# Kernel tuning notes

Measured on AMD Instinct MI355X. Metric: run time of the kernel, lower is better.

The kernel has to match this reference:

```python
import jax, jax.numpy as jnp
import numpy as np

H = 64          # hidden_size / SINDy latent dim
DM = 128        # d_model (GRU input size)
FF = 128        # dim_feedforward
NL = 2          # num_sindy_layers
EPS = 1e-5      # LayerNorm eps (torch default)
TRI_I, TRI_J = np.triu_indices(H)          # poly_order=2 pairs, torch loop order (i<=j)
LIB = 1 + H + TRI_I.size                   # 2145


def layernorm(x, g, b):
    m = jnp.mean(x, axis=-1, keepdims=True)
    v = jnp.mean((x - m) ** 2, axis=-1, keepdims=True)
    return (x - m) * jax.lax.rsqrt(v + EPS) * g + b


def sindy_library(z):
    # z: (N, H) -> Theta: (N, 1 + H + H*(H+1)/2); same term ordering as torch loops
    ones = jnp.ones((z.shape[0], 1), z.dtype)
    quad = z[:, TRI_I] * z[:, TRI_J]
    return jnp.concatenate([ones, z, quad], axis=1)


def gru_layer(x, Wih, Whh, bih, bhh):
    # x: (B, S, in), Wih: (3H, in), Whh: (3H, H); torch GRU gate order r,z,n
    xp = jnp.einsum('bsi,gi->bsg', x, Wih) + bih  # (B,S,3H) precomputed input projections
    B = x.shape[0]

    def step(h, xpt):
        gh = h @ Whh.T + bhh
        r = jax.nn.sigmoid(xpt[:, :H] + gh[:, :H])
        z = jax.nn.sigmoid(xpt[:, H:2 * H] + gh[:, H:2 * H])
        n = jnp.tanh(xpt[:, 2 * H:] + r * gh[:, 2 * H:])
        h = (1.0 - z) * n + z * h
        return h, h

    h0 = jnp.zeros((B, H), x.dtype)
    _, ys = jax.lax.scan(step, h0, jnp.swapaxes(xp, 0, 1))  # scan over time
    return jnp.swapaxes(ys, 0, 1)  # (B, S, H)


def sindy_layer(src, coef, g1, b1n, W1, bf1, W2, bf2, g2, b2n):
    B, S, _ = src.shape
    theta = sindy_library(src.reshape(-1, H))          # (N, LIB)
    upd = (theta @ coef).reshape(B, S, H)              # (B, S, H)
    src = layernorm(src + upd, g1, b1n)                # dropout = identity (eval)
    ff = jax.nn.gelu(src @ W1.T + bf1, approximate=False) @ W2.T + bf2
    return layernorm(src + ff, g2, b2n)


def setup_inputs() -> dict:
    key = jax.random.key(0)
    ks = jax.random.split(key, 24)
    f = lambda k, sh, s=0.05: (jax.random.normal(k, sh, dtype=jnp.float32) * s)
    inp = {
        'x': jax.random.normal(ks[0], (32, 500, DM), dtype=jnp.float32),
        # GRU layer 0 (input DM) and layer 1 (input H)
        'Wih0': f(ks[1], (3 * H, DM)), 'Whh0': f(ks[2], (3 * H, H)),
        'bih0': f(ks[3], (3 * H,)), 'bhh0': f(ks[4], (3 * H,)),
        'Wih1': f(ks[5], (3 * H, H)), 'Whh1': f(ks[6], (3 * H, H)),
        'bih1': f(ks[7], (3 * H,)), 'bhh1': f(ks[8], (3 * H,)),
        # stacked params for NL=2 identical SINDy layers
        'coeffs': f(ks[9], (NL, LIB, H), 0.02),
        'ln1_g': jnp.ones((NL, H), jnp.float32), 'ln1_b': jnp.zeros((NL, H), jnp.float32),
        'W1': f(ks[10], (NL, FF, H)), 'b1': f(ks[11], (NL, FF)),
        'W2': f(ks[12], (NL, H, FF)), 'b2': f(ks[13], (NL, H)),
        'ln2_g': jnp.ones((NL, H), jnp.float32), 'ln2_b': jnp.zeros((NL, H), jnp.float32),
    }
    return inp


def reference(x, Wih0, Whh0, bih0, bhh0, Wih1, Whh1, bih1, bhh1,
              coeffs, ln1_g, ln1_b, W1, b1, W2, b2, ln2_g, ln2_b):
    h = gru_layer(x, Wih0, Whh0, bih0, bhh0)
    h = gru_layer(h, Wih1, Whh1, bih1, bhh1)
    for l in range(NL):
        h = sindy_layer(h, coeffs[l], ln1_g[l], ln1_b[l], W1[l], b1[l],
                        W2[l], b2[l], ln2_g[l], ln2_b[l])
    return h, h[:, -1, :]
```

## Files before the change

### kernel.cpp

```cpp
#include <hip/hip_runtime.h>
#include <hip/hip_bf16.h>
#include <math.h>

#define H 64
#define DM 128
#define GDIM 192
#define BSZ 32
#define SEQ 500
#define NROW (BSZ*SEQ)
#define LIBN 2145
#define FFD 128
#define KPAD 2176
#define NKC 68

typedef __attribute__((ext_vector_type(8))) short short8;
typedef __attribute__((ext_vector_type(4))) float f32x4;
typedef __attribute__((ext_vector_type(4))) unsigned u32x4;

__device__ __forceinline__ float sigf(float x) {
    return 1.0f / (1.0f + __expf(-x));
}
__device__ __forceinline__ float tanhfast(float x) {
    x = fminf(fmaxf(x, -15.0f), 15.0f);
    float t = __expf(-2.0f * x);
    return (1.0f - t) / (1.0f + t);
}
__device__ __forceinline__ short bf16r(float f) {
    unsigned u = __float_as_uint(f);
    unsigned r = (u + 0x7fffu + ((u >> 16) & 1u)) >> 16;
    return (short)r;
}

__global__ void pack_wih0(const float* __restrict__ w, float* __restrict__ wt) {
    int idx = blockIdx.x * 256 + threadIdx.x;
    if (idx >= GDIM * DM) return;
    int e  = idx & 3;
    int g  = (idx >> 2) % GDIM;
    int k4 = idx / (GDIM * 4);
    wt[idx] = w[g * DM + k4 * 4 + e];
}

__global__ void pack_coef_frag(const float* __restrict__ coef, short* __restrict__ cp) {
    int idx = blockIdx.x * 256 + threadIdx.x;
    int j = idx & 7, lane = (idx >> 3) & 63, nt = (idx >> 9) & 3, kc = idx >> 11;
    int k = kc * 32 + ((lane >> 4) << 3) + j;
    int c = nt * 16 + (lane & 15);
    float v = (k < LIBN) ? coef[(size_t)k * H + c] : 0.0f;
    cp[idx] = bf16r(v);
}
__global__ void pack_w1_frag(const float* __restrict__ w1, short* __restrict__ wp) {
    int idx = blockIdx.x * 256 + threadIdx.x;
    int j = idx & 7, lane = (idx >> 3) & 63, nt = (idx >> 9) & 7, kc = idx >> 12;
    int k = kc * 32 + ((lane >> 4) << 3) + j;
    int n = nt * 16 + (lane & 15);
    wp[idx] = bf16r(w1[(size_t)n * H + k]);
}
__global__ void pack_w2_frag(const float* __restrict__ w2, short* __restrict__ wp) {
    int idx = blockIdx.x * 256 + threadIdx.x;
    int j = idx & 7, lane = (idx >> 3) & 63, nt = (idx >> 9) & 3, kc = idx >> 11;
    int k = kc * 32 + ((lane >> 4) << 3) + j;
    int n = nt * 16 + (lane & 15);
    wp[idx] = bf16r(w2[(size_t)n * FFD + k]);
}

__global__ __launch_bounds__(192, 2) void xp0_gemm(const float* __restrict__ x,
                                                   const float* __restrict__ wtp,
                                                   const float* __restrict__ bih0,
                                                   float* __restrict__ xp0) {
    __shared__ float xs[64][DM];
    int rb = blockIdx.x * 64;
    for (int idx = threadIdx.x; idx < 64 * 32; idx += 192) {
        int r = idx >> 5, k4 = idx & 31;
        ((f32x4*)xs[r])[k4] = ((const f32x4*)(x + (size_t)(rb + r) * DM))[k4];
    }
    __syncthreads();
    int g = threadIdx.x;
    float bias = bih0[g];
    float acc[64];
#pragma unroll
    for (int r = 0; r < 64; r++) acc[r] = bias;
    for (int k4 = 0; k4 < 32; k4++) {
        f32x4 w4 = ((const f32x4*)wtp)[k4 * GDIM + g];
#pragma unroll
        for (int r = 0; r < 64; r++) {
            f32x4 xv = ((f32x4*)xs[r])[k4];
            acc[r] += w4[0] * xv[0] + w4[1] * xv[1] + w4[2] * xv[2] + w4[3] * xv[3];
        }
    }
    for (int r = 0; r < 64; r++) xp0[(size_t)(rb + r) * GDIM + g] = acc[r];
}

__global__ __launch_bounds__(768, 3) void gru_fused(const float* __restrict__ xp0,
                                                    const float* __restrict__ whh0,
                                                    const float* __restrict__ bhh0,
                                                    const float* __restrict__ wih1,
                                                    const float* __restrict__ bih1,
                                                    const float* __restrict__ whh1,
                                                    const float* __restrict__ bhh1,
                                                    float* __restrict__ hbuf) {
    int b = blockIdx.x;
    int tid = threadIdx.x;
    int wv = __builtin_amdgcn_readfirstlane(tid >> 6);
    int lane = tid & 63;
    int m = wv % 3;
    int q = wv / 3;
    int k0 = q * 16;

    __shared__ __align__(16) float h0s[H];
    __shared__ __align__(16) float h1s[H];
    __shared__ float part[3][4][GDIM];

    if (tid < H) { h0s[tid] = 0.0f; h1s[tid] = 0.0f; }

    const float* W = (m == 0) ? whh0 : (m == 1) ? wih1 : whh1;
    float wr[16], wz[16], wn[16];
#pragma unroll
    for (int k4 = 0; k4 < 4; k4++) {
        f32x4 a = ((const f32x4*)(W + (size_t)lane * H + k0))[k4];
        f32x4 c = ((const f32x4*)(W + (size_t)(H + lane) * H + k0))[k4];
        f32x4 d = ((const f32x4*)(W + (size_t)(2 * H + lane) * H + k0))[k4];
        wr[4*k4] = a[0]; wr[4*k4+1] = a[1]; wr[4*k4+2] = a[2]; wr[4*k4+3] = a[3];
        wz[4*k4] = c[0]; wz[4*k4+1] = c[1]; wz[4*k4+2] = c[2]; wz[4*k4+3] = c[3];
        wn[4*k4] = d[0]; wn[4*k4+1] = d[1]; wn[4*k4+2] = d[2]; wn[4*k4+3] = d[3];
    }

    float b0r = 0, b0z = 0, b0n = 0;
    float b1ir = 0, b1iz = 0, b1in = 0, b1hr = 0, b1hz = 0, b1hn = 0;
    float hreg0 = 0.0f, hreg1 = 0.0f;
    const float* xpb = xp0 + (size_t)b * SEQ * GDIM;
    float xr_c = 0, xz_c = 0, xn_c = 0, xr_n = 0, xz_n = 0, xn_n = 0;
    if (wv == 0) {
        b0r = bhh0[lane]; b0z = bhh0[H + lane]; b0n = bhh0[2 * H + lane];
        xr_c = xpb[lane]; xz_c = xpb[H + lane]; xn_c = xpb[2 * H + lane];
    } else if (wv == 2) {
        b1ir = bih1[lane]; b1iz = bih1[H + lane]; b1in = bih1[2 * H + lane];
        b1hr = bhh1[lane]; b1hz = bhh1[H + lane]; b1hn = bhh1[2 * H + lane];
    }
    __syncthreads();

    for (int s = 0; s <= SEQ; s++) {
        if (wv == 0 && s + 1 < SEQ) {
            const float* p = xpb + (size_t)(s + 1) * GDIM;
            xr_n = p[lane]; xz_n = p[H + lane]; xn_n = p[2 * H + lane];
        }
        const float* hv = (m == 2) ? h1s : h0s;
        float ar = 0, az = 0, an = 0;
#pragma unroll
        for (int t4 = 0; t4 < 4; t4++) {
            f32x4 h4 = ((const f32x4*)(hv + k0))[t4];
            ar += wr[4*t4] * h4[0] + wr[4*t4+1] * h4[1] + wr[4*t4+2] * h4[2] + wr[4*t4+3] * h4[3];
            az += wz[4*t4] * h4[0] + wz[4*t4+1] * h4[1] + wz[4*t4+2] * h4[2] + wz[4*t4+3] * h4[3];
            an += wn[4*t4] * h4[0] + wn[4*t4+1] * h4[1] + wn[4*t4+2] * h4[2] + wn[4*t4+3] * h4[3];
        }
        part[m][q][lane] = ar;
        part[m][q][H + lane] = az;
        part[m][q][2 * H + lane] = an;
        __syncthreads();

        if (wv == 0) {
            if (s < SEQ) {
                float gr = b0r, gz = b0z, gn = b0n;
#pragma unroll
                for (int qq = 0; qq < 4; qq++) {
                    gr += part[0][qq][lane];
                    gz += part[0][qq][H + lane];
                    gn += part[0][qq][2 * H + lane];
                }
                float rg = sigf(xr_c + gr);
                float zg = sigf(xz_c + gz);
                float ng = tanhfast(xn_c + rg * gn);
                hreg0 = (1.0f - zg) * ng + zg * hreg0;
                h0s[lane] = hreg0;
                xr_c = xr_n; xz_c = xz_n; xn_c = xn_n;
            }
        } else if (wv == 2) {
            if (s >= 1) {
                float xr1 = b1ir, xz1 = b1iz, xn1 = b1in;
                float gr1 = b1hr, gz1 = b1hz, gn1 = b1hn;
#pragma unroll
                for (int qq = 0; qq < 4; qq++) {
                    xr1 += part[1][qq][lane];
                    xz1 += part[1][qq][H + lane];
                    xn1 += part[1][qq][2 * H + lane];
                    gr1 += part[2][qq][lane];
                    gz1 += part[2][qq][H + lane];
                    gn1 += part[2][qq][2 * H + lane];
                }
                float rg = sigf(xr1 + gr1);
                float zg = sigf(xz1 + gz1);
                float ng = tanhfast(xn1 + rg * gn1);
                hreg1 = (1.0f - zg) * ng + zg * hreg1;
                h1s[lane] = hreg1;
                hbuf[((size_t)b * SEQ + (s - 1)) * H + lane] = hreg1;
            }
        }
        __syncthreads();
    }
}

__global__ __launch_bounds__(512) void sindy_mfma(float* __restrict__ hbuf,
                                                  const short* __restrict__ cpk,
                                                  const short* __restrict__ w1p,
                                                  const short* __restrict__ w2p,
                                                  const float* __restrict__ g1,
                                                  const float* __restrict__ b1n,
                                                  const float* __restrict__ bf1,
                                                  const float* __restrict__ bf2v,
                                                  const float* __restrict__ g2,
                                                  const float* __restrict__ b2n,
                                                  float* __restrict__ out,
                                                  int final_layer) {
    __shared__ float z[64 * 68];
    __shared__ float upd[64 * 68];
    __shared__ float ff[64 * 132];
    __shared__ unsigned kmap[KPAD];
    __shared__ float bfs1[FFD], bfs2[H], g1s[H], b1s[H], g2s[H], b2s[H];

    int tid = threadIdx.x;
    int wv = __builtin_amdgcn_readfirstlane(tid >> 6);
    int lane = tid & 63;
    int row0 = blockIdx.x * 64;

    for (int idx = tid; idx < 64 * 16; idx += 512) {
        int r = idx >> 4, c4 = idx & 15;
        *(f32x4*)&z[r * 68 + c4 * 4] = *(const f32x4*)&hbuf[(size_t)(row0 + r) * H + c4 * 4];
    }
    for (int idx = tid; idx < 64 * 17; idx += 512)
        *(f32x4*)&upd[idx * 4] = (f32x4){0.f, 0.f, 0.f, 0.f};
    if (tid < 64) {
        z[tid * 68 + 64] = 1.0f; z[tid * 68 + 65] = 0.0f;
        z[tid * 68 + 66] = 0.0f; z[tid * 68 + 67] = 0.0f;
    }
    for (int k = tid; k < KPAD; k += 512) {
        unsigned a, b;
        if (k == 0) { a = 64; b = 64; }
        else if (k < 1 + H) { a = (unsigned)(k - 1); b = 64; }
        else if (k < LIBN) {
            int q = k - (1 + H);
            double s = sqrt(16641.0 - 8.0 * (double)q);
            int i = (int)((129.0 - s) * 0.5);
            int base = 64 * i - (i * (i - 1)) / 2;
            a = (unsigned)i; b = (unsigned)(i + (q - base));
        } else { a = 65; b = 65; }
        kmap[k] = (a << 16) | b;
    }
    if (tid < FFD) bfs1[tid] = bf1[tid];
    if (tid < H) {
        bfs2[tid] = bf2v[tid];
        g1s[tid] = g1[tid]; b1s[tid] = b1n[tid];
        g2s[tid] = g2[tid]; b2s[tid] = b2n[tid];
    }
    __syncthreads();

    int kj0 = ((lane >> 4) << 3);
    int m0 = (wv & 3) * 16;
    int m = m0 + (lane & 15);
    int rbase = m0 + ((lane >> 4) << 2);
    int cb16 = lane & 15;
    const float* zrow = &z[m * 68];

    {
        int p = wv >> 2;
        f32x4 acc[4] = {{0,0,0,0},{0,0,0,0},{0,0,0,0},{0,0,0,0}};
        for (int kc = p; kc < NKC; kc += 2) {
            int kbase = kc * 32 + kj0;
            u32x4 km0 = *(const u32x4*)&kmap[kbase];
            u32x4 km1 = *(const u32x4*)&kmap[kbase + 4];
            short8 af;
            af[0] = bf16r(zrow[km0[0] >> 16] * zrow[km0[0] & 0xffff]);
            af[1] = bf16r(zrow[km0[1] >> 16] * zrow[km0[1] & 0xffff]);
            af[2] = bf16r(zrow[km0[2] >> 16] * zrow[km0[2] & 0xffff]);
            af[3] = bf16r(zrow[km0[3] >> 16] * zrow[km0[3] & 0xffff]);
            af[4] = bf16r(zrow[km1[0] >> 16] * zrow[km1[0] & 0xffff]);
            af[5] = bf16r(zrow[km1[1] >> 16] * zrow[km1[1] & 0xffff]);
            af[6] = bf16r(zrow[km1[2] >> 16] * zrow[km1[2] & 0xffff]);
            af[7] = bf16r(zrow[km1[3] >> 16] * zrow[km1[3] & 0xffff]);
            const short* cb = cpk + ((size_t)(kc * 4) * 64 + lane) * 8;
#pragma unroll
            for (int nt = 0; nt < 4; nt++) {
                short8 bf = *(const short8*)(cb + (size_t)nt * 512);
                acc[nt] = __builtin_amdgcn_mfma_f32_16x16x32_bf16(af, bf, acc[nt], 0, 0, 0);
            }
        }
#pragma unroll
        for (int nt = 0; nt < 4; nt++)
#pragma unroll
            for (int r = 0; r < 4; r++)
                atomicAdd(&upd[(rbase + r) * 68 + nt * 16 + cb16], acc[nt][r]);
    }
    __syncthreads();

    if (wv == 0) {
        float v[64];
        float s1 = 0.0f;
#pragma unroll
        for (int c = 0; c < 64; c++) { v[c] = z[lane * 68 + c] + upd[lane * 68 + c]; s1 += v[c]; }
        float mn = s1 * (1.0f / 64.0f);
        float s2 = 0.0f;
#pragma unroll
        for (int c = 0; c < 64; c++) { float d = v[c] - mn; s2 += d * d; }
        float rstd = 1.0f / sqrtf(s2 * (1.0f / 64.0f) + 1e-5f);
#pragma unroll
        for (int c = 0; c < 64; c++)
            z[lane * 68 + c] = (v[c] - mn) * rstd * g1s[c] + b1s[c];
    }
    __syncthreads();

    {
        int nq = wv >> 2;
        f32x4 acc[4] = {{0,0,0,0},{0,0,0,0},{0,0,0,0},{0,0,0,0}};
#pragma unroll
        for (int kc = 0; kc < 2; kc++) {
            f32x4 za = *(const f32x4*)&z[m * 68 + kc * 32 + kj0];
            f32x4 zb = *(const f32x4*)&z[m * 68 + kc * 32 + kj0 + 4];
            short8 af;
            af[0] = bf16r(za[0]); af[1] = bf16r(za[1]); af[2] = bf16r(za[2]); af[3] = bf16r(za[3]);
            af[4] = bf16r(zb[0]); af[5] = bf16r(zb[1]); af[6] = bf16r(zb[2]); af[7] = bf16r(zb[3]);
#pragma unroll
            for (int t = 0; t < 4; t++) {
                int nt = nq * 4 + t;
                short8 bf = *(const short8*)(w1p + ((size_t)(kc * 8 + nt) * 64 + lane) * 8);
                acc[t] = __builtin_amdgcn_mfma_f32_16x16x32_bf16(af, bf, acc[t], 0, 0, 0);
            }
        }
#pragma unroll
        for (int t = 0; t < 4; t++) {
            int col = (nq * 4 + t) * 16 + cb16;
#pragma unroll
            for (int r = 0; r < 4; r++) {
                float v = acc[t][r] + bfs1[col];
                ff[(rbase + r) * 132 + col] = 0.5f * v * (1.0f + erff(v * 0.70710678118654752f));
            }
        }
    }
    __syncthreads();

    {
        int nh = wv >> 2;
        f32x4 acc[2] = {{0,0,0,0},{0,0,0,0}};
        const float* frow = &ff[m * 132];
#pragma unroll
        for (int kc = 0; kc < 4; kc++) {
            f32x4 fa = *(const f32x4*)&frow[kc * 32 + kj0];
            f32x4 fb = *(const f32x4*)&frow[kc * 32 + kj0 + 4];
            short8 af;
            af[0] = bf16r(fa[0]); af[1] = bf16r(fa[1]); af[2] = bf16r(fa[2]); af[3] = bf16r(fa[3]);
            af[4] = bf16r(fb[0]); af[5] = bf16r(fb[1]); af[6] = bf16r(fb[2]); af[7] = bf16r(fb[3]);
#pragma unroll
            for (int t = 0; t < 2; t++) {
                int nt = nh * 2 + t;
                short8 bf = *(const short8*)(w2p + ((size_t)(kc * 4 + nt) * 64 + lane) * 8);
                acc[t] = __builtin_amdgcn_mfma_f32_16x16x32_bf16(af, bf, acc[t], 0, 0, 0);
            }
        }
#pragma unroll
        for (int t = 0; t < 2; t++) {
            int col = (nh * 2 + t) * 16 + cb16;
#pragma unroll
            for (int r = 0; r < 4; r++)
                upd[(rbase + r) * 68 + col] = acc[t][r] + bfs2[col];
        }
    }
    __syncthreads();

    if (wv == 0) {
        float v[64];
        float s1 = 0.0f;
#pragma unroll
        for (int c = 0; c < 64; c++) { v[c] = z[lane * 68 + c] + upd[lane * 68 + c]; s1 += v[c]; }
        float mn = s1 * (1.0f / 64.0f);
        float s2 = 0.0f;
#pragma unroll
        for (int c = 0; c < 64; c++) { float d = v[c] - mn; s2 += d * d; }
        float rstd = 1.0f / sqrtf(s2 * (1.0f / 64.0f) + 1e-5f);
        int row = row0 + lane;
#pragma unroll
        for (int c = 0; c < 64; c++) {
            float res = (v[c] - mn) * rstd * g2s[c] + b2s[c];
            if (!final_layer) {
                hbuf[(size_t)row * H + c] = res;
            } else {
                out[(size_t)row * H + c] = res;
                if (row % SEQ == SEQ - 1)
                    out[(size_t)NROW * H + (row / SEQ) * H + c] = res;
            }
        }
    }
}

extern "C" void kernel_launch(void* const* d_in, const int* in_sizes, int n_in,
                              void* d_out, int out_size, void* d_ws, size_t ws_size,
                              hipStream_t stream) {
    const float* x    = (const float*)d_in[0];
    const float* wih0 = (const float*)d_in[1];
    const float* whh0 = (const float*)d_in[2];
    const float* bih0 = (const float*)d_in[3];
    const float* bhh0 = (const float*)d_in[4];
    const float* wih1 = (const float*)d_in[5];
    const float* whh1 = (const float*)d_in[6];
    const float* bih1 = (const float*)d_in[7];
    const float* bhh1 = (const float*)d_in[8];
    const float* coeffs = (const float*)d_in[9];
    const float* ln1g = (const float*)d_in[10];
    const float* ln1b = (const float*)d_in[11];
    const float* w1   = (const float*)d_in[12];
    const float* b1   = (const float*)d_in[13];
    const float* w2   = (const float*)d_in[14];
    const float* b2   = (const float*)d_in[15];
    const float* ln2g = (const float*)d_in[16];
    const float* ln2b = (const float*)d_in[17];

    float* out = (float*)d_out;
    float* ws  = (float*)d_ws;
    float* xp0 = ws;
    float* wtp = ws + (size_t)NROW * GDIM;
    short* bfa = (short*)(wtp + GDIM * DM);
    short* cpk[2] = { bfa, bfa + 139264 };
    short* w1pk[2] = { bfa + 2 * 139264, bfa + 2 * 139264 + 8192 };
    short* w2pk[2] = { bfa + 2 * 139264 + 2 * 8192, bfa + 2 * 139264 + 3 * 8192 };
    float* hbuf = out;

    pack_wih0<<<(GDIM * DM + 255) / 256, 256, 0, stream>>>(wih0, wtp);
    for (int l = 0; l < 2; l++) {
        pack_coef_frag<<<139264 / 256, 256, 0, stream>>>(coeffs + (size_t)l * LIBN * H, cpk[l]);
        pack_w1_frag<<<8192 / 256, 256, 0, stream>>>(w1 + (size_t)l * FFD * H, w1pk[l]);
        pack_w2_frag<<<8192 / 256, 256, 0, stream>>>(w2 + (size_t)l * H * FFD, w2pk[l]);
    }
    xp0_gemm<<<NROW / 64, 192, 0, stream>>>(x, wtp, bih0, xp0);
    gru_fused<<<BSZ, 768, 0, stream>>>(xp0, whh0, bhh0, wih1, bih1, whh1, bhh1, hbuf);
    for (int l = 0; l < 2; l++) {
        sindy_mfma<<<NROW / 64, 512, 0, stream>>>(
            hbuf, cpk[l], w1pk[l], w2pk[l],
            ln1g + l * H, ln1b + l * H, b1 + l * FFD,
            b2 + l * H, ln2g + l * H, ln2b + l * H,
            out, l == 1);
    }
}
```

Before: 573.0 us.

## Run GRU recurrence with bf16 MFMA over batches of 16 sequences per block

Replaces the per-sequence fp32 FMA GRU kernel (one block per batch element, 768 threads with partial-sum reduction through shared memory) with a kernel that batches 16 sequences per block and computes the recurrent matvecs as bf16 16x16x32 MFMAs. Weights are pre-packed into MFMA fragment layout, and hidden states are kept double-buffered in shared memory as bf16, which removes one barrier and the partial-sum reduction per step. The trade-off is only 2 blocks for the whole recurrence, so very low GPU occupancy, plus bf16 rounding of the hidden state feeding each step, which adds numerical error that accumulates over 500 steps.

```diff
diff --git a/kernel.cpp b/kernel.cpp
--- a/kernel.cpp
+++ b/kernel.cpp
@@ -12,6 +12,7 @@
 #define FFD 128
 #define KPAD 2176
 #define NKC 68
+#define NB 16
 
 typedef __attribute__((ext_vector_type(8))) short short8;
 typedef __attribute__((ext_vector_type(4))) float f32x4;
@@ -61,6 +62,14 @@
     int k = kc * 32 + ((lane >> 4) << 3) + j;
     int n = nt * 16 + (lane & 15);
     wp[idx] = bf16r(w2[(size_t)n * FFD + k]);
+}
+__global__ void pack_gruw_frag(const float* __restrict__ w, short* __restrict__ wp) {
+    int idx = blockIdx.x * 256 + threadIdx.x;
+    if (idx >= 12288) return;
+    int j = idx & 7, lane = (idx >> 3) & 63, kc = (idx >> 9) & 1, t = idx >> 10;
+    int m = 16 * t + (lane & 15);
+    int k = kc * 32 + ((lane >> 4) << 3) + j;
+    wp[idx] = bf16r(w[(size_t)m * H + k]);
 }
 
 __global__ __launch_bounds__(192, 2) void xp0_gemm(const float* __restrict__ x,
@@ -90,108 +99,137 @@
     for (int r = 0; r < 64; r++) xp0[(size_t)(rb + r) * GDIM + g] = acc[r];
 }
 
-__global__ __launch_bounds__(768, 3) void gru_fused(const float* __restrict__ xp0,
-                                                    const float* __restrict__ whh0,
-                                                    const float* __restrict__ bhh0,
-                                                    const float* __restrict__ wih1,
-                                                    const float* __restrict__ bih1,
-                                                    const float* __restrict__ whh1,
-                                                    const float* __restrict__ bhh1,
-                                                    float* __restrict__ hbuf) {
-    int b = blockIdx.x;
+__global__ __launch_bounds__(512) void gru_mfma(const float* __restrict__ xp0,
+                                                const short* __restrict__ a0,
+                                                const short* __restrict__ a1,
+                                                const short* __restrict__ a2,
+                                                const float* __restrict__ bhh0,
+                                                const float* __restrict__ bih1,
+                                                const float* __restrict__ bhh1,
+                                                float* __restrict__ hbuf) {
+    int n0 = blockIdx.x * NB;
     int tid = threadIdx.x;
     int wv = __builtin_amdgcn_readfirstlane(tid >> 6);
     int lane = tid & 63;
-    int m = wv % 3;
-    int q = wv / 3;
-    int k0 = q * 16;
-
-    __shared__ __align__(16) float h0s[H];
-    __shared__ __align__(16) float h1s[H];
-    __shared__ float part[3][4][GDIM];
-
-    if (tid < H) { h0s[tid] = 0.0f; h1s[tid] = 0.0f; }
-
-    const float* W = (m == 0) ? whh0 : (m == 1) ? wih1 : whh1;
-    float wr[16], wz[16], wn[16];
-#pragma unroll
-    for (int k4 = 0; k4 < 4; k4++) {
-        f32x4 a = ((const f32x4*)(W + (size_t)lane * H + k0))[k4];
-        f32x4 c = ((const f32x4*)(W + (size_t)(H + lane) * H + k0))[k4];
-        f32x4 d = ((const f32x4*)(W + (size_t)(2 * H + lane) * H + k0))[k4];
-        wr[4*k4] = a[0]; wr[4*k4+1] = a[1]; wr[4*k4+2] = a[2]; wr[4*k4+3] = a[3];
-        wz[4*k4] = c[0]; wz[4*k4+1] = c[1]; wz[4*k4+2] = c[2]; wz[4*k4+3] = c[3];
-        wn[4*k4] = d[0]; wn[4*k4+1] = d[1]; wn[4*k4+2] = d[2]; wn[4*k4+3] = d[3];
-    }
-
-    float b0r = 0, b0z = 0, b0n = 0;
-    float b1ir = 0, b1iz = 0, b1in = 0, b1hr = 0, b1hz = 0, b1hn = 0;
-    float hreg0 = 0.0f, hreg1 = 0.0f;
-    const float* xpb = xp0 + (size_t)b * SEQ * GDIM;
-    float xr_c = 0, xz_c = 0, xn_c = 0, xr_n = 0, xz_n = 0, xn_n = 0;
-    if (wv == 0) {
-        b0r = bhh0[lane]; b0z = bhh0[H + lane]; b0n = bhh0[2 * H + lane];
-        xr_c = xpb[lane]; xz_c = xpb[H + lane]; xn_c = xpb[2 * H + lane];
-    } else if (wv == 2) {
-        b1ir = bih1[lane]; b1iz = bih1[H + lane]; b1in = bih1[2 * H + lane];
-        b1hr = bhh1[lane]; b1hz = bhh1[H + lane]; b1hn = bhh1[2 * H + lane];
+    int g = wv >> 2;
+    int w = wv & 3;
+    int quad = lane >> 4;
+    int n = lane & 15;
+    int i0 = 16 * w + quad * 4;
+
+    __shared__ short hb0[2][NB][72];
+    __shared__ short hb1[2][NB][72];
+
+    for (int idx = tid; idx < 2 * NB * 72; idx += 512) {
+        ((short*)hb0)[idx] = 0;
+        ((short*)hb1)[idx] = 0;
+    }
+
+    short8 A0[6], A1[6], A2[6];
+    if (g == 0) {
+#pragma unroll
+        for (int t3 = 0; t3 < 3; t3++)
+#pragma unroll
+            for (int kc = 0; kc < 2; kc++)
+                A0[t3 * 2 + kc] = *(const short8*)(a0 + (((size_t)(w + 4 * t3) * 2 + kc) * 64 + lane) * 8);
+    } else {
+#pragma unroll
+        for (int t3 = 0; t3 < 3; t3++)
+#pragma unroll
+            for (int kc = 0; kc < 2; kc++) {
+                A1[t3 * 2 + kc] = *(const short8*)(a1 + (((size_t)(w + 4 * t3) * 2 + kc) * 64 + lane) * 8);
+                A2[t3 * 2 + kc] = *(const short8*)(a2 + (((size_t)(w + 4 * t3) * 2 + kc) * 64 + lane) * 8);
+            }
+    }
+    float bR[4], bZ[4], bN[4], cR[4], cZ[4], cN[4];
+#pragma unroll
+    for (int r = 0; r < 4; r++) {
+        if (g == 0) {
+            bR[r] = bhh0[i0 + r]; bZ[r] = bhh0[H + i0 + r]; bN[r] = bhh0[2 * H + i0 + r];
+        } else {
+            bR[r] = bih1[i0 + r]; bZ[r] = bih1[H + i0 + r]; bN[r] = bih1[2 * H + i0 + r];
+            cR[r] = bhh1[i0 + r]; cZ[r] = bhh1[H + i0 + r]; cN[r] = bhh1[2 * H + i0 + r];
+        }
+    }
+
+    float hprev[4] = {0.f, 0.f, 0.f, 0.f};
+    const float* xpB = xp0 + (size_t)(n0 + n) * SEQ * GDIM;
+    f32x4 xr_c = {0,0,0,0}, xz_c = {0,0,0,0}, xn_c = {0,0,0,0};
+    f32x4 xr_n = {0,0,0,0}, xz_n = {0,0,0,0}, xn_n = {0,0,0,0};
+    if (g == 0) {
+        xr_c = *(const f32x4*)(xpB + i0);
+        xz_c = *(const f32x4*)(xpB + H + i0);
+        xn_c = *(const f32x4*)(xpB + 2 * H + i0);
     }
     __syncthreads();
 
     for (int s = 0; s <= SEQ; s++) {
-        if (wv == 0 && s + 1 < SEQ) {
-            const float* p = xpb + (size_t)(s + 1) * GDIM;
-            xr_n = p[lane]; xz_n = p[H + lane]; xn_n = p[2 * H + lane];
-        }
-        const float* hv = (m == 2) ? h1s : h0s;
-        float ar = 0, az = 0, an = 0;
-#pragma unroll
-        for (int t4 = 0; t4 < 4; t4++) {
-            f32x4 h4 = ((const f32x4*)(hv + k0))[t4];
-            ar += wr[4*t4] * h4[0] + wr[4*t4+1] * h4[1] + wr[4*t4+2] * h4[2] + wr[4*t4+3] * h4[3];
-            az += wz[4*t4] * h4[0] + wz[4*t4+1] * h4[1] + wz[4*t4+2] * h4[2] + wz[4*t4+3] * h4[3];
-            an += wn[4*t4] * h4[0] + wn[4*t4+1] * h4[1] + wn[4*t4+2] * h4[2] + wn[4*t4+3] * h4[3];
-        }
-        part[m][q][lane] = ar;
-        part[m][q][H + lane] = az;
-        part[m][q][2 * H + lane] = an;
-        __syncthreads();
-
-        if (wv == 0) {
+        int rp = s & 1, wp = (s + 1) & 1;
+        if (g == 0 && s + 1 < SEQ) {
+            const float* p = xpB + (size_t)(s + 1) * GDIM;
+            xr_n = *(const f32x4*)(p + i0);
+            xz_n = *(const f32x4*)(p + H + i0);
+            xn_n = *(const f32x4*)(p + 2 * H + i0);
+        }
+        short8 B0k0 = *(const short8*)&hb0[rp][n][quad * 8];
+        short8 B0k1 = *(const short8*)&hb0[rp][n][32 + quad * 8];
+
+        if (g == 0) {
+            f32x4 aR = {0,0,0,0}, aZ = {0,0,0,0}, aN = {0,0,0,0};
+            aR = __builtin_amdgcn_mfma_f32_16x16x32_bf16(A0[0], B0k0, aR, 0, 0, 0);
+            aR = __builtin_amdgcn_mfma_f32_16x16x32_bf16(A0[1], B0k1, aR, 0, 0, 0);
+            aZ = __builtin_amdgcn_mfma_f32_16x16x32_bf16(A0[2], B0k0, aZ, 0, 0, 0);
+            aZ = __builtin_amdgcn_mfma_f32_16x16x32_bf16(A0[3], B0k1, aZ, 0, 0, 0);
+            aN = __builtin_amdgcn_mfma_f32_16x16x32_bf16(A0[4], B0k0, aN, 0, 0, 0);
+            aN = __builtin_amdgcn_mfma_f32_16x16x32_bf16(A0[5], B0k1, aN, 0, 0, 0);
             if (s < SEQ) {
-                float gr = b0r, gz = b0z, gn = b0n;
-#pragma unroll
-                for (int qq = 0; qq < 4; qq++) {
-                    gr += part[0][qq][lane];
-                    gz += part[0][qq][H + lane];
-                    gn += part[0][qq][2 * H + lane];
+                short hq[4];
+#pragma unroll
+                for (int r = 0; r < 4; r++) {
+                    float rg = sigf(xr_c[r] + aR[r] + bR[r]);
+                    float zg = sigf(xz_c[r] + aZ[r] + bZ[r]);
+                    float ng = tanhfast(xn_c[r] + rg * (aN[r] + bN[r]));
+                    hprev[r] = (1.0f - zg) * ng + zg * hprev[r];
+                    hq[r] = bf16r(hprev[r]);
                 }
-                float rg = sigf(xr_c + gr);
-                float zg = sigf(xz_c + gz);
-                float ng = tanhfast(xn_c + rg * gn);
-                hreg0 = (1.0f - zg) * ng + zg * hreg0;
-                h0s[lane] = hreg0;
+                unsigned lo = ((unsigned)(unsigned short)hq[0]) | (((unsigned)(unsigned short)hq[1]) << 16);
+                unsigned hi = ((unsigned)(unsigned short)hq[2]) | (((unsigned)(unsigned short)hq[3]) << 16);
+                *(uint2*)&hb0[wp][n][i0] = make_uint2(lo, hi);
                 xr_c = xr_n; xz_c = xz_n; xn_c = xn_n;
             }
-        } else if (wv == 2) {
+        } else {
+            short8 B1k0 = *(const short8*)&hb1[rp][n][quad * 8];
+            short8 B1k1 = *(const short8*)&hb1[rp][n][32 + quad * 8];
+            f32x4 aIr = {0,0,0,0}, aIz = {0,0,0,0}, aIn = {0,0,0,0};
+            f32x4 aHr = {0,0,0,0}, aHz = {0,0,0,0}, aHn = {0,0,0,0};
+            aIr = __builtin_amdgcn_mfma_f32_16x16x32_bf16(A1[0], B0k0, aIr, 0, 0, 0);
+            aIr = __builtin_amdgcn_mfma_f32_16x16x32_bf16(A1[1], B0k1, aIr, 0, 0, 0);
+            aIz = __builtin_amdgcn_mfma_f32_16x16x32_bf16(A1[2], B0k0, aIz, 0, 0, 0);
+            aIz = __builtin_amdgcn_mfma_f32_16x16x32_bf16(A1[3], B0k1, aIz, 0, 0, 0);
+            aIn = __builtin_amdgcn_mfma_f32_16x16x32_bf16(A1[4], B0k0, aIn, 0, 0, 0);
+            aIn = __builtin_amdgcn_mfma_f32_16x16x32_bf16(A1[5], B0k1, aIn, 0, 0, 0);
+            aHr = __builtin_amdgcn_mfma_f32_16x16x32_bf16(A2[0], B1k0, aHr, 0, 0, 0);
+            aHr = __builtin_amdgcn_mfma_f32_16x16x32_bf16(A2[1], B1k1, aHr, 0, 0, 0);
+            aHz = __builtin_amdgcn_mfma_f32_16x16x32_bf16(A2[2], B1k0, aHz, 0, 0, 0);
+            aHz = __builtin_amdgcn_mfma_f32_16x16x32_bf16(A2[3], B1k1, aHz, 0, 0, 0);
+            aHn = __builtin_amdgcn_mfma_f32_16x16x32_bf16(A2[4], B1k0, aHn, 0, 0, 0);
+            aHn = __builtin_amdgcn_mfma_f32_16x16x32_bf16(A2[5], B1k1, aHn, 0, 0, 0);
             if (s >= 1) {
-                float xr1 = b1ir, xz1 = b1iz, xn1 = b1in;
-                float gr1 = b1hr, gz1 = b1hz, gn1 = b1hn;
-#pragma unroll
-                for (int qq = 0; qq < 4; qq++) {
-                    xr1 += part[1][qq][lane];
-                    xz1 += part[1][qq][H + lane];
-                    xn1 += part[1][qq][2 * H + lane];
-                    gr1 += part[2][qq][lane];
-                    gz1 += part[2][qq][H + lane];
-                    gn1 += part[2][qq][2 * H + lane];
+                short hq[4];
+                f32x4 hv;
+#pragma unroll
+                for (int r = 0; r < 4; r++) {
+                    float rg = sigf(aIr[r] + bR[r] + aHr[r] + cR[r]);
+                    float zg = sigf(aIz[r] + bZ[r] + aHz[r] + cZ[r]);
+                    float ng = tanhfast(aIn[r] + bN[r] + rg * (aHn[r] + cN[r]));
+                    hprev[r] = (1.0f - zg) * ng + zg * hprev[r];
+                    hq[r] = bf16r(hprev[r]);
+                    hv[r] = hprev[r];
                 }
-                float rg = sigf(xr1 + gr1);
-                float zg = sigf(xz1 + gz1);
-                float ng = tanhfast(xn1 + rg * gn1);
-                hreg1 = (1.0f - zg) * ng + zg * hreg1;
-                h1s[lane] = hreg1;
-                hbuf[((size_t)b * SEQ + (s - 1)) * H + lane] = hreg1;
+                unsigned lo = ((unsigned)(unsigned short)hq[0]) | (((unsigned)(unsigned short)hq[1]) << 16);
+                unsigned hi = ((unsigned)(unsigned short)hq[2]) | (((unsigned)(unsigned short)hq[3]) << 16);
+                *(uint2*)&hb1[wp][n][i0] = make_uint2(lo, hi);
+                *(f32x4*)&hbuf[((size_t)(n0 + n) * SEQ + (s - 1)) * H + i0] = hv;
             }
         }
         __syncthreads();
@@ -418,6 +456,9 @@
     short* cpk[2] = { bfa, bfa + 139264 };
     short* w1pk[2] = { bfa + 2 * 139264, bfa + 2 * 139264 + 8192 };
     short* w2pk[2] = { bfa + 2 * 139264 + 2 * 8192, bfa + 2 * 139264 + 3 * 8192 };
+    short* ga0 = bfa + 2 * 139264 + 4 * 8192;
+    short* ga1 = ga0 + 12288;
+    short* ga2 = ga1 + 12288;
     float* hbuf = out;
 
     pack_wih0<<<(GDIM * DM + 255) / 256, 256, 0, stream>>>(wih0, wtp);
@@ -426,8 +467,11 @@
         pack_w1_frag<<<8192 / 256, 256, 0, stream>>>(w1 + (size_t)l * FFD * H, w1pk[l]);
         pack_w2_frag<<<8192 / 256, 256, 0, stream>>>(w2 + (size_t)l * H * FFD, w2pk[l]);
     }
+    pack_gruw_frag<<<48, 256, 0, stream>>>(whh0, ga0);
+    pack_gruw_frag<<<48, 256, 0, stream>>>(wih1, ga1);
+    pack_gruw_frag<<<48, 256, 0, stream>>>(whh1, ga2);
     xp0_gemm<<<NROW / 64, 192, 0, stream>>>(x, wtp, bih0, xp0);
-    gru_fused<<<BSZ, 768, 0, stream>>>(xp0, whh0, bhh0, wih1, bih1, whh1, bhh1, hbuf);
+    gru_mfma<<<BSZ / NB, 512, 0, stream>>>(xp0, ga0, ga1, ga2, bhh0, bih1, bhh1, hbuf);
     for (int l = 0; l < 2; l++) {
         sindy_mfma<<<NROW / 64, 512, 0, stream>>>(
             hbuf, cpk[l], w1pk[l], w2pk[l],
```

Result: slower. 804.6 us (+40.4%).

## Interleave GRU input projections in 4-step chunks and prefetch two chunks ahead

Applied to the files above, without the earlier changes.

xp0_gemm now writes the layer-0 input projections transposed into [batch][chunk of 4 steps][gate][4] order, so each lane of the GRU wave fetches four timesteps with one 16-byte load. Loads are prefetched two to three chunks ahead through a four-slot register ring. The GRU time loop is unrolled into 4-step chunks so hbuf stores are batched four steps at a time. The aim is to take global-load latency off the serial recurrence's critical path, at the cost of more registers and a scattered write pattern in the GEMM epilogue.

```diff
diff --git a/kernel.cpp b/kernel.cpp
--- a/kernel.cpp
+++ b/kernel.cpp
@@ -66,7 +66,7 @@
 __global__ __launch_bounds__(192, 2) void xp0_gemm(const float* __restrict__ x,
                                                    const float* __restrict__ wtp,
                                                    const float* __restrict__ bih0,
-                                                   float* __restrict__ xp0) {
+                                                   float* __restrict__ xpT) {
     __shared__ float xs[64][DM];
     int rb = blockIdx.x * 64;
     for (int idx = threadIdx.x; idx < 64 * 32; idx += 192) {
@@ -87,10 +87,15 @@
             acc[r] += w4[0] * xv[0] + w4[1] * xv[1] + w4[2] * xv[2] + w4[3] * xv[3];
         }
     }
-    for (int r = 0; r < 64; r++) xp0[(size_t)(rb + r) * GDIM + g] = acc[r];
-}
-
-__global__ __launch_bounds__(768, 3) void gru_fused(const float* __restrict__ xp0,
+    for (int r = 0; r < 64; r++) {
+        int row = rb + r;
+        int bb = row / 500;
+        int ss = row - bb * 500;
+        xpT[(((size_t)bb * 125 + (ss >> 2)) * GDIM + g) * 4 + (ss & 3)] = acc[r];
+    }
+}
+
+__global__ __launch_bounds__(768, 3) void gru_fused(const float* __restrict__ xpT,
                                                     const float* __restrict__ whh0,
                                                     const float* __restrict__ bhh0,
                                                     const float* __restrict__ wih1,
@@ -127,22 +132,32 @@
     float b0r = 0, b0z = 0, b0n = 0;
     float b1ir = 0, b1iz = 0, b1in = 0, b1hr = 0, b1hz = 0, b1hn = 0;
     float hreg0 = 0.0f, hreg1 = 0.0f;
-    const float* xpb = xp0 + (size_t)b * SEQ * GDIM;
-    float xr_c = 0, xz_c = 0, xn_c = 0, xr_n = 0, xz_n = 0, xn_n = 0;
+    float hb4[4] = {0.f, 0.f, 0.f, 0.f};
+    f32x4 xc[4][3];
+    const float* xpB = xpT + (size_t)b * 125 * GDIM * 4;
+
     if (wv == 0) {
         b0r = bhh0[lane]; b0z = bhh0[H + lane]; b0n = bhh0[2 * H + lane];
-        xr_c = xpb[lane]; xz_c = xpb[H + lane]; xn_c = xpb[2 * H + lane];
+#pragma unroll
+        for (int g3 = 0; g3 < 3; g3++) {
+            xc[0][g3] = *(const f32x4*)(xpB + ((size_t)0 * GDIM + g3 * 64 + lane) * 4);
+            xc[1][g3] = *(const f32x4*)(xpB + ((size_t)1 * GDIM + g3 * 64 + lane) * 4);
+        }
     } else if (wv == 2) {
         b1ir = bih1[lane]; b1iz = bih1[H + lane]; b1in = bih1[2 * H + lane];
         b1hr = bhh1[lane]; b1hz = bhh1[H + lane]; b1hn = bhh1[2 * H + lane];
     }
     __syncthreads();
 
-    for (int s = 0; s <= SEQ; s++) {
-        if (wv == 0 && s + 1 < SEQ) {
-            const float* p = xpb + (size_t)(s + 1) * GDIM;
-            xr_n = p[lane]; xz_n = p[H + lane]; xn_n = p[2 * H + lane];
-        }
+    auto loadch = [&](int c, int buf) {
+        if (c < 125) {
+#pragma unroll
+            for (int g3 = 0; g3 < 3; g3++)
+                xc[buf][g3] = *(const f32x4*)(xpB + ((size_t)c * GDIM + g3 * 64 + lane) * 4);
+        }
+    };
+
+    auto step = [&](int s, int e, float xr, float xz, float xn) {
         const float* hv = (m == 2) ? h1s : h0s;
         float ar = 0, az = 0, an = 0;
 #pragma unroll
@@ -166,12 +181,11 @@
                     gz += part[0][qq][H + lane];
                     gn += part[0][qq][2 * H + lane];
                 }
-                float rg = sigf(xr_c + gr);
-                float zg = sigf(xz_c + gz);
-                float ng = tanhfast(xn_c + rg * gn);
+                float rg = sigf(xr + gr);
+                float zg = sigf(xz + gz);
+                float ng = tanhfast(xn + rg * gn);
                 hreg0 = (1.0f - zg) * ng + zg * hreg0;
                 h0s[lane] = hreg0;
-                xr_c = xr_n; xz_c = xz_n; xn_c = xn_n;
             }
         } else if (wv == 2) {
             if (s >= 1) {
@@ -191,11 +205,39 @@
                 float ng = tanhfast(xn1 + rg * gn1);
                 hreg1 = (1.0f - zg) * ng + zg * hreg1;
                 h1s[lane] = hreg1;
-                hbuf[((size_t)b * SEQ + (s - 1)) * H + lane] = hreg1;
+                hb4[(e + 3) & 3] = hreg1;
+                if (e == 0) {
+                    float* dst = hbuf + ((size_t)b * SEQ + (s - 4)) * H + lane;
+#pragma unroll
+                    for (int t = 0; t < 4; t++) dst[t * H] = hb4[t];
+                }
             }
         }
         __syncthreads();
-    }
+    };
+
+    for (int scb = 0; scb < 31; scb++) {
+#pragma unroll
+        for (int sci = 0; sci < 4; sci++) {
+            int sc = scb * 4 + sci;
+            if (wv == 0 && (sci & 1) == 0) {
+                loadch(sc + 2, (sci + 2) & 3);
+                loadch(sc + 3, (sci + 3) & 3);
+            }
+            int s0 = sc * 4;
+            step(s0 + 0, 0, xc[sci][0][0], xc[sci][1][0], xc[sci][2][0]);
+            step(s0 + 1, 1, xc[sci][0][1], xc[sci][1][1], xc[sci][2][1]);
+            step(s0 + 2, 2, xc[sci][0][2], xc[sci][1][2], xc[sci][2][2]);
+            step(s0 + 3, 3, xc[sci][0][3], xc[sci][1][3], xc[sci][2][3]);
+        }
+    }
+    {
+        step(496, 0, xc[0][0][0], xc[0][1][0], xc[0][2][0]);
+        step(497, 1, xc[0][0][1], xc[0][1][1], xc[0][2][1]);
+        step(498, 2, xc[0][0][2], xc[0][1][2], xc[0][2][2]);
+        step(499, 3, xc[0][0][3], xc[0][1][3], xc[0][2][3]);
+    }
+    step(500, 0, 0.0f, 0.0f, 0.0f);
 }
 
 __global__ __launch_bounds__(512) void sindy_mfma(float* __restrict__ hbuf,
@@ -236,11 +278,11 @@
         if (k == 0) { a = 64; b = 64; }
         else if (k < 1 + H) { a = (unsigned)(k - 1); b = 64; }
         else if (k < LIBN) {
-            int q = k - (1 + H);
-            double s = sqrt(16641.0 - 8.0 * (double)q);
+            int qq = k - (1 + H);
+            double s = sqrt(16641.0 - 8.0 * (double)qq);
             int i = (int)((129.0 - s) * 0.5);
             int base = 64 * i - (i * (i - 1)) / 2;
-            a = (unsigned)i; b = (unsigned)(i + (q - base));
+            a = (unsigned)i; b = (unsigned)(i + (qq - base));
         } else { a = 65; b = 65; }
         kmap[k] = (a << 16) | b;
     }
@@ -412,7 +454,7 @@
 
     float* out = (float*)d_out;
     float* ws  = (float*)d_ws;
-    float* xp0 = ws;
+    float* xpT = ws;
     float* wtp = ws + (size_t)NROW * GDIM;
     short* bfa = (short*)(wtp + GDIM * DM);
     short* cpk[2] = { bfa, bfa + 139264 };
@@ -426,8 +468,8 @@
         pack_w1_frag<<<8192 / 256, 256, 0, stream>>>(w1 + (size_t)l * FFD * H, w1pk[l]);
         pack_w2_frag<<<8192 / 256, 256, 0, stream>>>(w2 + (size_t)l * H * FFD, w2pk[l]);
     }
-    xp0_gemm<<<NROW / 64, 192, 0, stream>>>(x, wtp, bih0, xp0);
-    gru_fused<<<BSZ, 768, 0, stream>>>(xp0, whh0, bhh0, wih1, bih1, whh1, bhh1, hbuf);
+    xp0_gemm<<<NROW / 64, 192, 0, stream>>>(x, wtp, bih0, xpT);
+    gru_fused<<<BSZ, 768, 0, stream>>>(xpT, whh0, bhh0, wih1, bih1, whh1, bhh1, hbuf);
     for (int l = 0; l < 2; l++) {
         sindy_mfma<<<NROW / 64, 512, 0, stream>>>(
             hbuf, cpk[l], w1pk[l], w2pk[l],
```

Measured after the change: 553.4 us. 1.04x faster.
